# Kernel optimization log

Hardware: AMD Instinct MI355X
Metric: run time of the kernel (lower is better)

The kernel has to match this reference:

```python
import jax, jax.numpy as jnp
import numpy as np

TEMP = 16.0  # sqrt(in_dim=256), module default when temperature=None
BN_EPS = 1e-5


def setup_inputs() -> dict:
    key = jax.random.key(0)
    ks = jax.random.split(key, 8)
    B, Cin, T, H, W = 8, 256, 8, 16, 16
    FF, Cout = 512, 256
    # small init scale keeps softmax logits in a sane range
    s = 0.02
    return {
        "x": jax.random.normal(ks[0], (B, Cin, T, H, W), jnp.float32),
        "Wk": jax.random.normal(ks[1], (FF, Cin), jnp.float32) * s,
        "Wq": jax.random.normal(ks[2], (FF, Cin), jnp.float32) * s,
        "Wv": jax.random.normal(ks[3], (FF, Cin), jnp.float32) * s,
        "Wout": jax.random.normal(ks[4], (Cout, FF), jnp.float32) * s,
        "bout": jax.random.normal(ks[5], (Cout,), jnp.float32) * s,
        "gamma": jnp.ones((Cout,), jnp.float32),
        "beta": jnp.zeros((Cout,), jnp.float32),
    }


def reference(x, Wk, Wq, Wv, Wout, bout, gamma, beta):
    B, Cin, T, H, W = x.shape
    N = T * H * W
    xf = x.reshape(B, Cin, N)                      # 1x1x1 conv == per-position matmul
    K = jnp.einsum('fc,bcn->bfn', Wk, xf)
    Q = jnp.einsum('fc,bcn->bfn', Wq, xf)
    V = jnp.einsum('fc,bcn->bfn', Wv, xf)
    KQ = jnp.einsum('bfi,bfj->bij', K, Q)          # [B, N, N] = K^T Q
    attn = jax.nn.softmax(KQ / TEMP, axis=2)
    # torch: sum(V[:, :, :, None] * attn[:, None], dim=3)
    #      = V[b,c,i] * sum_j attn[b,i,j]  (no need to materialize B x C x N x N)
    agg = V * jnp.sum(attn, axis=2)[:, None, :]    # [B, FF, N]
    o = jnp.einsum('of,bfn->bon', Wout, agg) + bout[None, :, None]
    o = jax.nn.relu(o).reshape(B, -1, T, H, W)
    y = x + o                                      # residual (in_dim == out_dim)
    # BatchNorm3d, training mode (fresh module): batch stats over (B, T, H, W)
    mean = jnp.mean(y, axis=(0, 2, 3, 4), keepdims=True)
    var = jnp.var(y, axis=(0, 2, 3, 4), keepdims=True)
    g = gamma[None, :, None, None, None]
    b = beta[None, :, None, None, None]
    return g * (y - mean) * jax.lax.rsqrt(var + BN_EPS) + b
```

## Files before the change

### kernel.cpp

```cpp
#include <hip/hip_runtime.h>

typedef __attribute__((ext_vector_type(8))) short short8;
typedef __attribute__((ext_vector_type(4))) float floatx4;

#define CIN  256
#define NSP  2048
#define COUT 256

__device__ __forceinline__ unsigned short f2bf_rne(float f) {
  unsigned int u = __float_as_uint(f);
  u += 0x7fffu + ((u >> 16) & 1u);
  return (unsigned short)(u >> 16);
}

__device__ __forceinline__ unsigned int pack_bf16_hu(float lo, float hi) {
  unsigned int a = __float_as_uint(lo) + 0x8000u;
  unsigned int b = __float_as_uint(hi) + 0x8000u;
  return __builtin_amdgcn_perm(b, a, 0x07060302u);
}

__global__ __launch_bounds__(1024) void k1_m(
    const float* __restrict__ Wv, const float* __restrict__ Wout,
    unsigned short* __restrict__ Mb, float* __restrict__ stats)
{
  __shared__ float ws[512];
  __shared__ float red[4][256];
  const int tid = threadIdx.x;
  const int r   = blockIdx.x;
  if (r == 0 && tid < 512) stats[tid] = 0.f;
  if (tid < 512) ws[tid] = Wout[(size_t)r * 512 + tid];
  __syncthreads();
  const int c  = tid & 255;
  const int fs = tid >> 8;
  float acc = 0.f;
  #pragma unroll 16
  for (int f0 = 0; f0 < 128; ++f0) {
    int f = fs * 128 + f0;
    acc += ws[f] * Wv[(size_t)f * 256 + c];
  }
  red[fs][c] = acc;
  __syncthreads();
  if (tid < 256) {
    float s = red[0][tid] + red[1][tid] + red[2][tid] + red[3][tid];
    Mb[(size_t)r * 256 + tid] = f2bf_rne(s);
  }
}

__global__ __launch_bounds__(256) void k2_gemm(
    const float* __restrict__ x, const unsigned short* __restrict__ Mb,
    const float* __restrict__ bout, float* __restrict__ stats,
    float* __restrict__ out)
{
  __shared__ float ls[128], lq[128];
  const int tid  = threadIdx.x;
  const int lane = tid & 63;
  const int wave = tid >> 6;
  const int m16  = lane & 15;
  const int q    = lane >> 4;
  const int nb   = blockIdx.x * 64;
  const int ocb  = blockIdx.y * 128;
  const int b    = blockIdx.z;
  const int wocb = ocb + (wave & 1) * 64;
  const int wnb  = nb + (wave >> 1) * 32;

  if (tid < 128) { ls[tid] = 0.f; lq[tid] = 0.f; }

  floatx4 acc[4][2];
  #pragma unroll
  for (int i = 0; i < 4; ++i)
    #pragma unroll
    for (int j = 0; j < 2; ++j)
      acc[i][j] = (floatx4){0.f, 0.f, 0.f, 0.f};

  const unsigned short* Ab = Mb + (size_t)(wocb + m16) * 256 + q * 8;
  const float* xb = x + (size_t)b * CIN * NSP;
  const float* Bb = xb + (size_t)(q * 8) * NSP + wnb + m16;

  #pragma unroll
  for (int kk = 0; kk < 8; ++kk) {
    short8 av[4];
    #pragma unroll
    for (int ti = 0; ti < 4; ++ti)
      av[ti] = *(const short8*)(Ab + (size_t)ti * 16 * 256 + kk * 32);
    short8 bv[2];
    #pragma unroll
    for (int tj = 0; tj < 2; ++tj) {
      const float* bp = Bb + (size_t)(kk * 32) * NSP + tj * 16;
      union { unsigned int u[4]; short8 v; } p;
      #pragma unroll
      for (int j = 0; j < 4; ++j) {
        float f0 = bp[(size_t)(2 * j) * NSP];
        float f1 = bp[(size_t)(2 * j + 1) * NSP];
        p.u[j] = pack_bf16_hu(f0, f1);
      }
      bv[tj] = p.v;
    }
    #pragma unroll
    for (int ti = 0; ti < 4; ++ti)
      #pragma unroll
      for (int tj = 0; tj < 2; ++tj)
        acc[ti][tj] = __builtin_amdgcn_mfma_f32_16x16x32_bf16(av[ti], bv[tj], acc[ti][tj], 0, 0, 0);
  }

  __syncthreads();

  #pragma unroll
  for (int ti = 0; ti < 4; ++ti) {
    #pragma unroll
    for (int r = 0; r < 4; ++r) {
      const int ocl = (wave & 1) * 64 + ti * 16 + q * 4 + r;
      const int oc  = ocb + ocl;
      const float bo = bout[oc];
      float s = 0.f, s2 = 0.f;
      #pragma unroll
      for (int tj = 0; tj < 2; ++tj) {
        const int n = wnb + tj * 16 + m16;
        const size_t gidx = ((size_t)(b * COUT + oc)) * NSP + n;
        float o = fmaxf(acc[ti][tj][r] + bo, 0.f);
        float y = x[gidx] + o;
        out[gidx] = y;
        s += y;
        s2 += y * y;
      }
      #pragma unroll
      for (int d = 1; d < 16; d <<= 1) {
        s  += __shfl_xor(s, d, 64);
        s2 += __shfl_xor(s2, d, 64);
      }
      if (m16 == 0) {
        atomicAdd(&ls[ocl], s);
        atomicAdd(&lq[ocl], s2);
      }
    }
  }
  __syncthreads();
  if (tid < 128) {
    atomicAdd(&stats[ocb + tid], ls[tid]);
    atomicAdd(&stats[256 + ocb + tid], lq[tid]);
  }
}

__global__ __launch_bounds__(256) void k3_norm(
    const float* __restrict__ stats, const float* __restrict__ gamma,
    const float* __restrict__ beta, float* __restrict__ out)
{
  const int row = blockIdx.x;
  const int oc  = row & 255;
  const float inv_n = 1.f / 16384.f;
  const float m  = stats[oc] * inv_n;
  const float v  = stats[256 + oc] * inv_n - m * m;
  const float sc = gamma[oc] * rsqrtf(v + 1e-5f);
  const float sh = beta[oc] - m * sc;
  float* p = out + (size_t)row * 2048 + threadIdx.x * 8;
  float4 a = *(const float4*)p;
  float4 c = *(const float4*)(p + 4);
  a.x = a.x * sc + sh; a.y = a.y * sc + sh;
  a.z = a.z * sc + sh; a.w = a.w * sc + sh;
  c.x = c.x * sc + sh; c.y = c.y * sc + sh;
  c.z = c.z * sc + sh; c.w = c.w * sc + sh;
  *(float4*)p = a;
  *(float4*)(p + 4) = c;
}

extern "C" void kernel_launch(void* const* d_in, const int* in_sizes, int n_in,
                              void* d_out, int out_size, void* d_ws, size_t ws_size,
                              hipStream_t stream) {
  const float* x     = (const float*)d_in[0];
  const float* Wv    = (const float*)d_in[3];
  const float* Wout  = (const float*)d_in[4];
  const float* bout  = (const float*)d_in[5];
  const float* gamma = (const float*)d_in[6];
  const float* beta  = (const float*)d_in[7];
  float* out = (float*)d_out;

  char* w = (char*)d_ws;
  unsigned short* Mb = (unsigned short*)w;
  float* stats = (float*)(w + 131072);

  hipLaunchKernelGGL(k1_m,    dim3(256),       dim3(1024), 0, stream,
                     Wv, Wout, Mb, stats);
  hipLaunchKernelGGL(k2_gemm, dim3(32, 2, 8),  dim3(256),  0, stream,
                     x, Mb, bout, stats, out);
  hipLaunchKernelGGL(k3_norm, dim3(2048),      dim3(256),  0, stream,
                     stats, gamma, beta, out);
}
```

Baseline: 114.2 us.

## Fuse weight-product, GEMM and batchnorm into one cooperative kernel with grid syncs

Replaces the three kernel launches with a single cooperative kernel of 512 blocks. The first 256 blocks compute the folded bf16 weight matrix Wout·Wv, followed by a grid sync. The GEMM then keeps the residual output in registers, accumulates BN statistics, and after a second grid sync applies the normalization directly from registers. This removes two launches and the intermediate write and re-read of the output tensor. The costs are two grid-wide barriers, a weight-product stage that uses only 256 threads per row, and a dependence on all 512 blocks being co-resident.

```diff
diff --git a/kernel.cpp b/kernel.cpp
--- a/kernel.cpp
+++ b/kernel.cpp
@@ -1,4 +1,7 @@
 #include <hip/hip_runtime.h>
+#include <hip/hip_cooperative_groups.h>
+
+namespace cg = cooperative_groups;
 
 typedef __attribute__((ext_vector_type(8))) short short8;
 typedef __attribute__((ext_vector_type(4))) float floatx4;
@@ -6,6 +9,10 @@
 #define CIN  256
 #define NSP  2048
 #define COUT 256
+#define FF   512
+
+__device__ unsigned short g_M[COUT * CIN];
+__device__ float g_stats[2 * COUT];
 
 __device__ __forceinline__ unsigned short f2bf_rne(float f) {
   unsigned int u = __float_as_uint(f);
@@ -19,40 +26,32 @@
   return __builtin_amdgcn_perm(b, a, 0x07060302u);
 }
 
-__global__ __launch_bounds__(1024) void k1_m(
-    const float* __restrict__ Wv, const float* __restrict__ Wout,
-    unsigned short* __restrict__ Mb, float* __restrict__ stats)
-{
-  __shared__ float ws[512];
-  __shared__ float red[4][256];
-  const int tid = threadIdx.x;
-  const int r   = blockIdx.x;
-  if (r == 0 && tid < 512) stats[tid] = 0.f;
-  if (tid < 512) ws[tid] = Wout[(size_t)r * 512 + tid];
-  __syncthreads();
-  const int c  = tid & 255;
-  const int fs = tid >> 8;
-  float acc = 0.f;
-  #pragma unroll 16
-  for (int f0 = 0; f0 < 128; ++f0) {
-    int f = fs * 128 + f0;
-    acc += ws[f] * Wv[(size_t)f * 256 + c];
-  }
-  red[fs][c] = acc;
-  __syncthreads();
-  if (tid < 256) {
-    float s = red[0][tid] + red[1][tid] + red[2][tid] + red[3][tid];
-    Mb[(size_t)r * 256 + tid] = f2bf_rne(s);
-  }
-}
-
-__global__ __launch_bounds__(256) void k2_gemm(
-    const float* __restrict__ x, const unsigned short* __restrict__ Mb,
-    const float* __restrict__ bout, float* __restrict__ stats,
+__global__ __launch_bounds__(256, 2) void fused_all(
+    const float* __restrict__ x, const float* __restrict__ Wv,
+    const float* __restrict__ Wout, const float* __restrict__ bout,
+    const float* __restrict__ gamma, const float* __restrict__ beta,
     float* __restrict__ out)
 {
   __shared__ float ls[128], lq[128];
-  const int tid  = threadIdx.x;
+  const int tid = threadIdx.x;
+  const int bid = blockIdx.x + 32 * (blockIdx.y + 2 * blockIdx.z);
+
+  if (tid < 128) { ls[tid] = 0.f; lq[tid] = 0.f; }
+
+  if (bid < 256) {
+    const float* wo = Wout + (size_t)bid * FF;
+    float accm = 0.f;
+    #pragma unroll 16
+    for (int f = 0; f < FF; ++f)
+      accm += wo[f] * Wv[(size_t)f * 256 + tid];
+    g_M[bid * 256 + tid] = f2bf_rne(accm);
+  } else if (bid == 256) {
+    g_stats[tid] = 0.f;
+    g_stats[256 + tid] = 0.f;
+  }
+
+  cg::this_grid().sync();
+
   const int lane = tid & 63;
   const int wave = tid >> 6;
   const int m16  = lane & 15;
@@ -63,8 +62,6 @@
   const int wocb = ocb + (wave & 1) * 64;
   const int wnb  = nb + (wave >> 1) * 32;
 
-  if (tid < 128) { ls[tid] = 0.f; lq[tid] = 0.f; }
-
   floatx4 acc[4][2];
   #pragma unroll
   for (int i = 0; i < 4; ++i)
@@ -72,7 +69,7 @@
     for (int j = 0; j < 2; ++j)
       acc[i][j] = (floatx4){0.f, 0.f, 0.f, 0.f};
 
-  const unsigned short* Ab = Mb + (size_t)(wocb + m16) * 256 + q * 8;
+  const unsigned short* Ab = g_M + (size_t)(wocb + m16) * 256 + q * 8;
   const float* xb = x + (size_t)b * CIN * NSP;
   const float* Bb = xb + (size_t)(q * 8) * NSP + wnb + m16;
 
@@ -102,8 +99,6 @@
         acc[ti][tj] = __builtin_amdgcn_mfma_f32_16x16x32_bf16(av[ti], bv[tj], acc[ti][tj], 0, 0, 0);
   }
 
-  __syncthreads();
-
   #pragma unroll
   for (int ti = 0; ti < 4; ++ti) {
     #pragma unroll
@@ -118,7 +113,7 @@
         const size_t gidx = ((size_t)(b * COUT + oc)) * NSP + n;
         float o = fmaxf(acc[ti][tj][r] + bo, 0.f);
         float y = x[gidx] + o;
-        out[gidx] = y;
+        acc[ti][tj][r] = y;
         s += y;
         s2 += y * y;
       }
@@ -135,31 +130,31 @@
   }
   __syncthreads();
   if (tid < 128) {
-    atomicAdd(&stats[ocb + tid], ls[tid]);
-    atomicAdd(&stats[256 + ocb + tid], lq[tid]);
+    atomicAdd(&g_stats[ocb + tid], ls[tid]);
+    atomicAdd(&g_stats[256 + ocb + tid], lq[tid]);
   }
-}
 
-__global__ __launch_bounds__(256) void k3_norm(
-    const float* __restrict__ stats, const float* __restrict__ gamma,
-    const float* __restrict__ beta, float* __restrict__ out)
-{
-  const int row = blockIdx.x;
-  const int oc  = row & 255;
+  cg::this_grid().sync();
+
   const float inv_n = 1.f / 16384.f;
-  const float m  = stats[oc] * inv_n;
-  const float v  = stats[256 + oc] * inv_n - m * m;
-  const float sc = gamma[oc] * rsqrtf(v + 1e-5f);
-  const float sh = beta[oc] - m * sc;
-  float* p = out + (size_t)row * 2048 + threadIdx.x * 8;
-  float4 a = *(const float4*)p;
-  float4 c = *(const float4*)(p + 4);
-  a.x = a.x * sc + sh; a.y = a.y * sc + sh;
-  a.z = a.z * sc + sh; a.w = a.w * sc + sh;
-  c.x = c.x * sc + sh; c.y = c.y * sc + sh;
-  c.z = c.z * sc + sh; c.w = c.w * sc + sh;
-  *(float4*)p = a;
-  *(float4*)(p + 4) = c;
+  #pragma unroll
+  for (int ti = 0; ti < 4; ++ti) {
+    #pragma unroll
+    for (int r = 0; r < 4; ++r) {
+      const int ocl = (wave & 1) * 64 + ti * 16 + q * 4 + r;
+      const int oc  = ocb + ocl;
+      const float m  = g_stats[oc] * inv_n;
+      const float v  = g_stats[256 + oc] * inv_n - m * m;
+      const float sc = gamma[oc] * rsqrtf(v + 1e-5f);
+      const float sh = beta[oc] - m * sc;
+      #pragma unroll
+      for (int tj = 0; tj < 2; ++tj) {
+        const int n = wnb + tj * 16 + m16;
+        const size_t gidx = ((size_t)(b * COUT + oc)) * NSP + n;
+        out[gidx] = acc[ti][tj][r] * sc + sh;
+      }
+    }
+  }
 }
 
 extern "C" void kernel_launch(void* const* d_in, const int* in_sizes, int n_in,
@@ -173,14 +168,8 @@
   const float* beta  = (const float*)d_in[7];
   float* out = (float*)d_out;
 
-  char* w = (char*)d_ws;
-  unsigned short* Mb = (unsigned short*)w;
-  float* stats = (float*)(w + 131072);
-
-  hipLaunchKernelGGL(k1_m,    dim3(256),       dim3(1024), 0, stream,
-                     Wv, Wout, Mb, stats);
-  hipLaunchKernelGGL(k2_gemm, dim3(32, 2, 8),  dim3(256),  0, stream,
-                     x, Mb, bout, stats, out);
-  hipLaunchKernelGGL(k3_norm, dim3(2048),      dim3(256),  0, stream,
-                     stats, gamma, beta, out);
+  void* args[] = { (void*)&x, (void*)&Wv, (void*)&Wout, (void*)&bout,
+                   (void*)&gamma, (void*)&beta, (void*)&out };
+  hipLaunchCooperativeKernel(fused_all, dim3(32, 2, 8), dim3(256),
+                             args, 0, stream);
 }
```

Result: slower. 248.8 us (+117.9%).
